# Optimization experiments

Measured on AMD Instinct MI355X. Metric: run time of the kernel, lower is better.

## Reference

```python
import jax, jax.numpy as jnp
import numpy as np

S = 32          # input grid resolution
N = 2048        # active input voxels
C = 256         # in channels
CO = 128        # out channels
S2 = 2 * S      # upsampled resolution
M = 8 * N       # candidate child voxels
EPS = 1e-6


def setup_inputs() -> dict:
    key = jax.random.key(0)
    ks = jax.random.split(key, 8)
    # unique voxel coordinates (sparse occupancy)
    lin = jax.random.permutation(ks[0], S ** 3)[:N]
    coords = jnp.stack([lin // (S * S), (lin // S) % S, lin % S], axis=-1).astype(jnp.int32)
    sc = 0.05
    return {
        "feats": jax.random.normal(ks[1], (N, C), jnp.float32),
        "norm1_w": 1.0 + 0.1 * jax.random.normal(ks[2], (C,), jnp.float32),
        "norm1_b": 0.1 * jax.random.normal(ks[3], (C,), jnp.float32),
        "subdiv_w": sc * jax.random.normal(ks[4], (C, 8), jnp.float32),
        "subdiv_b": jnp.zeros((8,), jnp.float32),
        "conv1_w": sc * jax.random.normal(ks[5], (27, C, CO), jnp.float32),
        "conv1_b": jnp.zeros((CO,), jnp.float32),
        "conv2_w": sc * jax.random.normal(ks[6], (27, CO, CO), jnp.float32),
        "conv2_b": jnp.zeros((CO,), jnp.float32),
        "skip_w": sc * jax.random.normal(ks[7], (C, CO), jnp.float32),
        "skip_b": jnp.zeros((CO,), jnp.float32),
        "coords": coords,
    }


def _layernorm(x, w=None, b=None):
    # LayerNorm32: fp32 math, eps=1e-6
    m = jnp.mean(x, axis=-1, keepdims=True)
    v = jnp.var(x, axis=-1, keepdims=True)
    y = (x - m) * jax.lax.rsqrt(v + EPS)
    if w is not None:
        y = y * w + b
    return y


def _sparse_conv(feats, nidx, w, b):
    # submanifold 3x3x3 sparse conv: gather 27 neighbors, contract.
    # nidx: [M,27] with sentinel M pointing at a zero row.
    pad = jnp.concatenate([feats, jnp.zeros((1, feats.shape[1]), feats.dtype)], axis=0)
    g = pad[nidx]                                   # [M, 27, Cin]
    return jnp.einsum('nkc,kcd->nd', g, w) + b


def _forward(feats, norm1_w, norm1_b, subdiv_w, subdiv_b, conv1_w, conv1_b,
             conv2_w, conv2_b, skip_w, skip_b, coords):
    # subdiv prediction (SparseLinear C -> 8)
    subdiv = feats @ subdiv_w + subdiv_b            # [N, 8]
    # norm1 + silu
    h = jax.nn.silu(_layernorm(feats, norm1_w, norm1_b))
    # sparse upsample x2 with octree subdivision mask
    mask = (subdiv > 0).reshape(-1)                 # [M]
    j = jnp.arange(8, dtype=jnp.int32)
    offs8 = jnp.stack([(j >> 2) & 1, (j >> 1) & 1, j & 1], axis=-1)  # [8,3]
    cc = (coords[:, None, :] * 2 + offs8[None]).reshape(-1, 3)        # [M,3]
    h_c = jnp.where(mask[:, None], jnp.repeat(h, 8, axis=0), 0.0)     # [M,C]
    x_c = jnp.where(mask[:, None], jnp.repeat(feats, 8, axis=0), 0.0)
    # neighbor lookup grid (padded by 1; default M -> zero feature row)
    grid = jnp.full((S2 + 2, S2 + 2, S2 + 2), M, jnp.int32)
    grid = grid.at[cc[:, 0] + 1, cc[:, 1] + 1, cc[:, 2] + 1].set(
        jnp.arange(M, dtype=jnp.int32))
    d = jnp.arange(-1, 2, dtype=jnp.int32)
    offs27 = jnp.stack(jnp.meshgrid(d, d, d, indexing='ij'), axis=-1).reshape(27, 3)
    nc = cc[:, None, :] + 1 + offs27[None]          # [M,27,3]
    nidx = grid[nc[..., 0], nc[..., 1], nc[..., 2]] # [M,27]
    # conv1 -> norm2 (no affine) -> silu -> conv2
    h1 = jax.nn.silu(_layernorm(_sparse_conv(h_c, nidx, conv1_w, conv1_b)))
    h2 = _sparse_conv(h1, nidx, conv2_w, conv2_b)
    # residual with linear skip; mask out non-subdivided children
    out = (h2 + x_c @ skip_w + skip_b) * mask[:, None].astype(h2.dtype)
    return out, subdiv


def reference(feats, norm1_w, norm1_b, subdiv_w, subdiv_b, conv1_w, conv1_b,
              conv2_w, conv2_b, skip_w, skip_b, coords):
    return _forward(feats, norm1_w, norm1_b, subdiv_w, subdiv_b, conv1_w,
                    conv1_b, conv2_w, conv2_b, skip_w, skip_b, coords)
```

## Files before the change

kernel.cpp:

```cpp
#include <hip/hip_runtime.h>
#include <cstdint>
#include <cstddef>

constexpr int N  = 2048;
constexpr int C  = 256;
constexpr int CO = 128;
constexpr int M  = 16384;
constexpr int G  = 66;
constexpr int KP = 6;
constexpr int KCHUNK = 5;
constexpr float EPS = 1e-6f;

using bf8 = __attribute__((ext_vector_type(8))) short;
using f4  = __attribute__((ext_vector_type(4))) float;

static __device__ __forceinline__ unsigned short f2bf(float f) {
  unsigned u = __float_as_uint(f);
  u += 0x7fffu + ((u >> 16) & 1u);
  return (unsigned short)(u >> 16);
}
static __device__ __forceinline__ float bf2f(unsigned short s) {
  return __uint_as_float((unsigned)s << 16);
}

__global__ __launch_bounds__(256) void k_prep(
    const float* __restrict__ c1w, unsigned short* __restrict__ w1t,
    const float* __restrict__ c2w, unsigned short* __restrict__ w2t,
    int* __restrict__ grid, unsigned short* __restrict__ h,
    unsigned short* __restrict__ h1) {
  int i = blockIdx.x * 256 + threadIdx.x;
  if (i < G * G * G) grid[i] = M;
  if (blockIdx.x == 1200) {
    if (threadIdx.x < C) h[(size_t)N * C + threadIdx.x] = 0;
  }
  if (blockIdx.x == 1201) {
    if (threadIdx.x < CO) h1[(size_t)M * CO + threadIdx.x] = 0;
  }

  __shared__ float tile[32][33];
  int bx = blockIdx.x;
  const float* w; unsigned short* wtp; int cin, k, cb, ob;
  if (bx < 864) {
    w = c1w; wtp = w1t; cin = C;
    k = bx >> 5; int tl = bx & 31; cb = tl >> 2; ob = tl & 3;
  } else {
    int b2 = bx - 864;
    w = c2w; wtp = w2t; cin = CO;
    k = b2 >> 4; int tl = b2 & 15; cb = tl >> 2; ob = tl & 3;
  }
  int ty = threadIdx.x >> 5, tx = threadIdx.x & 31;
#pragma unroll
  for (int j = 0; j < 4; ++j) {
    int row = ty + j * 8;
    tile[row][tx] = w[((size_t)k * cin + cb * 32 + row) * CO + ob * 32 + tx];
  }
  __syncthreads();
#pragma unroll
  for (int j = 0; j < 4; ++j) {
    int row = ty + j * 8;
    wtp[((size_t)k * CO + ob * 32 + row) * cin + cb * 32 + tx] =
        f2bf(tile[tx][row]);
  }
}

__global__ __launch_bounds__(256) void k_rownorm(
    const float* __restrict__ feats, const float* __restrict__ n1w,
    const float* __restrict__ n1b, const float* __restrict__ sdw,
    const float* __restrict__ sdb, float* __restrict__ out_subdiv,
    unsigned short* __restrict__ h, int* __restrict__ pidx,
    float* __restrict__ maskf, const int* __restrict__ coords,
    int* __restrict__ grid, const float* __restrict__ skw,
    const float* __restrict__ skb, float* __restrict__ sres) {
  int n = blockIdx.x, t = threadIdx.x;
  __shared__ float sx[256];
  __shared__ float sacc[256];
  float x = feats[(size_t)n * C + t];
  sx[t] = x;
  float4 w0 = *(const float4*)(sdw + t * 8);
  float4 w1 = *(const float4*)(sdw + t * 8 + 4);
  float v[10] = {x * w0.x, x * w0.y, x * w0.z, x * w0.w,
                 x * w1.x, x * w1.y, x * w1.z, x * w1.w, x, x * x};
#pragma unroll
  for (int mk = 1; mk < 64; mk <<= 1) {
#pragma unroll
    for (int j = 0; j < 10; ++j) v[j] += __shfl_xor(v[j], mk, 64);
  }
  __shared__ float red[4][10];
  int wave = t >> 6, lane = t & 63;
  if (lane == 0) {
#pragma unroll
    for (int j = 0; j < 10; ++j) red[wave][j] = v[j];
  }
  __syncthreads();
  float sums[10];
#pragma unroll
  for (int j = 0; j < 10; ++j)
    sums[j] = red[0][j] + red[1][j] + red[2][j] + red[3][j];
  float mean = sums[8] / (float)C;
  float var  = sums[9] / (float)C - mean * mean;
  float rstd = rsqrtf(var + EPS);
  if (t < 8) {
    float sd = sums[t] + sdb[t];
    out_subdiv[(size_t)n * 8 + t] = sd;
    bool mk = sd > 0.f;
    pidx[n * 8 + t]  = mk ? n : N;
    maskf[n * 8 + t] = mk ? 1.f : 0.f;
    int xx = coords[n * 3 + 0] * 2 + ((t >> 2) & 1) + 1;
    int yy = coords[n * 3 + 1] * 2 + ((t >> 1) & 1) + 1;
    int zz = coords[n * 3 + 2] * 2 + (t & 1) + 1;
    grid[(xx * G + yy) * G + zz] = n * 8 + t;
  }
  float y  = (x - mean) * rstd * n1w[t] + n1b[t];
  float sl = y / (1.f + __expf(-y));
  h[(size_t)n * C + t] = f2bf(sl);

  int o = t & 127, half = t >> 7;
  const float* wp = skw + (size_t)(half * 128) * CO + o;
  const float* xs = sx + half * 128;
  float a = 0.f;
#pragma unroll 8
  for (int c = 0; c < 128; ++c) a += xs[c] * wp[(size_t)c * CO];
  sacc[t] = a;
  __syncthreads();
  if (t < 128) sres[(size_t)n * CO + t] = sacc[t] + sacc[t + 128] + skb[t];
}

template <int CIN, int NCB, bool UP>
__global__ __launch_bounds__(256, 3) void k_conv(
    const unsigned short* __restrict__ src, const int* __restrict__ coords,
    const int* __restrict__ grid, const int* __restrict__ pidx,
    const unsigned short* __restrict__ wt, unsigned short* __restrict__ part) {
  __shared__ unsigned short sB[2][128 * 32];
  const int t = threadIdx.x;
  const int w = t >> 6, lane = t & 63;
  const int quad = lane >> 4, ln = lane & 15;
  const int m0 = blockIdx.x * 128;
  const int kpart = blockIdx.y;
  const int k0 = kpart * KCHUNK;
  const int nk = min(KCHUNK, 27 - k0);
  const int nstage = nk * NCB;
  const int rh = (w >> 1) * 64, ch = (w & 1) * 64;

  const int row2 = t >> 1;
  const int c0 = (t & 1) * 2;
  const int x3 = (row2 >> 1) & 3;
  const int wsl0 = row2 * 32 + ((c0) ^ x3) * 8;
  const int wsl1 = row2 * 32 + ((c0 + 1) ^ x3) * 8;
  const int slot = (quad ^ ((ln >> 1) & 3)) * 8;

  int gb[4];
#pragma unroll
  for (int ti = 0; ti < 4; ++ti) {
    int m = m0 + rh + ti * 16 + ln;
    int p = m >> 3, j = m & 7;
    int cx = coords[p * 3 + 0] * 2 + ((j >> 2) & 1) + 1;
    int cy = coords[p * 3 + 1] * 2 + ((j >> 1) & 1) + 1;
    int cz = coords[p * 3 + 2] * 2 + (j & 1) + 1;
    gb[ti] = (cx * G + cy) * G + cz;
  }
  auto tapoff = [&](int k) {
    return (k / 9 - 1) * (G * G) + ((k / 3) % 3 - 1) * G + (k % 3 - 1);
  };
  auto lookup = [&](int ti, int doff) {
    int g = grid[gb[ti] + doff];
    if (UP) return (g >= M) ? N : pidx[g & (M - 1)];
    return g;
  };

  bf8 rb0, rb1;
  bf8 ra[4], rn[4];
  int ga[4], gn[4];

  auto loadB = [&](int s) {
    const int kk = s / NCB, cb = s - kk * NCB;
    const unsigned short* pb =
        wt + ((size_t)(k0 + kk) * CO + row2) * CIN + cb * 32 + c0 * 8;
    rb0 = *(const bf8*)(pb);
    rb1 = *(const bf8*)(pb + 8);
  };
  auto writeB = [&](int buf) {
    *(bf8*)(sB[buf] + wsl0) = rb0;
    *(bf8*)(sB[buf] + wsl1) = rb1;
  };

  f4 acc[16];
  f4 zero = {0.f, 0.f, 0.f, 0.f};
#pragma unroll
  for (int i = 0; i < 16; ++i) acc[i] = zero;

  {
    int d0 = tapoff(k0);
#pragma unroll
    for (int ti = 0; ti < 4; ++ti) ga[ti] = lookup(ti, d0);
  }
  loadB(0);
#pragma unroll
  for (int ti = 0; ti < 4; ++ti)
    ra[ti] = *(const bf8*)(src + (size_t)ga[ti] * CIN + quad * 8);
  writeB(0);

  for (int s = 0; s < nstage; ++s) {
    const int buf = s & 1;
    const int kk = s / NCB, cb = s - kk * NCB;
    const bool have = (s + 1 < nstage);
    if (cb == 0 && kk + 1 < nk) {
      int dn = tapoff(k0 + kk + 1);
#pragma unroll
      for (int ti = 0; ti < 4; ++ti) gn[ti] = lookup(ti, dn);
    }
    if (have) {
      loadB(s + 1);
      const int cb1 = (cb + 1 < NCB) ? cb + 1 : 0;
      const int* gu = (cb + 1 < NCB) ? ga : gn;
#pragma unroll
      for (int ti = 0; ti < 4; ++ti)
        rn[ti] = *(const bf8*)(src + (size_t)gu[ti] * CIN + cb1 * 32 + quad * 8);
    }
    __syncthreads();
    const unsigned short* pb = sB[buf];
    bf8 bv[4];
#pragma unroll
    for (int tj = 0; tj < 4; ++tj)
      bv[tj] = *(const bf8*)(pb + (ch + tj * 16 + ln) * 32 + slot);
#pragma unroll
    for (int ti = 0; ti < 4; ++ti)
#pragma unroll
      for (int tj = 0; tj < 4; ++tj)
        acc[ti * 4 + tj] = __builtin_amdgcn_mfma_f32_16x16x32_bf16(
            ra[ti], bv[tj], acc[ti * 4 + tj], 0, 0, 0);
    if (have) {
      writeB(buf ^ 1);
#pragma unroll
      for (int ti = 0; ti < 4; ++ti) ra[ti] = rn[ti];
      if (cb + 1 == NCB) {
#pragma unroll
        for (int ti = 0; ti < 4; ++ti) ga[ti] = gn[ti];
      }
    }
  }

  unsigned short* pp = part + ((size_t)kpart * M + m0) * CO;
#pragma unroll
  for (int ti = 0; ti < 4; ++ti) {
    int mrow = rh + ti * 16 + quad * 4;
#pragma unroll
    for (int tj = 0; tj < 4; ++tj) {
      int co = ch + tj * 16 + ln;
#pragma unroll
      for (int rr = 0; rr < 4; ++rr)
        pp[(size_t)(mrow + rr) * CO + co] = f2bf(acc[ti * 4 + tj][rr]);
    }
  }
}

__global__ __launch_bounds__(256) void k_r1(const unsigned short* __restrict__ p,
                                            const float* __restrict__ bias,
                                            unsigned short* __restrict__ h1) {
  int wave = threadIdx.x >> 6, lane = threadIdx.x & 63;
  int m = blockIdx.x * 4 + wave;
  float v0 = bias[lane], v1 = bias[lane + 64];
#pragma unroll
  for (int q = 0; q < KP; ++q) {
    const unsigned short* pq = p + ((size_t)q * M + m) * CO;
    v0 += bf2f(pq[lane]);
    v1 += bf2f(pq[lane + 64]);
  }
  float sum = v0 + v1, sq = v0 * v0 + v1 * v1;
#pragma unroll
  for (int mk = 1; mk < 64; mk <<= 1) {
    sum += __shfl_xor(sum, mk, 64);
    sq  += __shfl_xor(sq, mk, 64);
  }
  float mean = sum / (float)CO;
  float var  = sq / (float)CO - mean * mean;
  float rstd = rsqrtf(var + EPS);
  float y0 = (v0 - mean) * rstd;
  float y1 = (v1 - mean) * rstd;
  float s0 = y0 / (1.f + __expf(-y0));
  float s1 = y1 / (1.f + __expf(-y1));
  h1[(size_t)m * CO + lane]      = f2bf(s0);
  h1[(size_t)m * CO + lane + 64] = f2bf(s1);
}

__global__ __launch_bounds__(256) void k_r2(const unsigned short* __restrict__ p,
                                            const float* __restrict__ bias,
                                            const float* __restrict__ sres,
                                            const float* __restrict__ maskf,
                                            float* __restrict__ out) {
  int i = blockIdx.x * 256 + threadIdx.x;
  int m = i >> 5;
  int o4 = (i & 31) * 4;
  float4 acc = *(const float4*)(bias + o4);
#pragma unroll
  for (int q = 0; q < KP; ++q) {
    ushort4 a = *(const ushort4*)(p + ((size_t)q * M + m) * CO + o4);
    acc.x += bf2f(a.x); acc.y += bf2f(a.y);
    acc.z += bf2f(a.z); acc.w += bf2f(a.w);
  }
  float4 s = *(const float4*)(sres + (size_t)(m >> 3) * CO + o4);
  float mk = maskf[m];
  float4 r;
  r.x = (acc.x + s.x) * mk;
  r.y = (acc.y + s.y) * mk;
  r.z = (acc.z + s.z) * mk;
  r.w = (acc.w + s.w) * mk;
  *(float4*)(out + (size_t)m * CO + o4) = r;
}

extern "C" void kernel_launch(void* const* d_in, const int* in_sizes, int n_in,
                              void* d_out, int out_size, void* d_ws, size_t ws_size,
                              hipStream_t stream) {
  const float* feats = (const float*)d_in[0];
  const float* n1w   = (const float*)d_in[1];
  const float* n1b   = (const float*)d_in[2];
  const float* sdw   = (const float*)d_in[3];
  const float* sdb   = (const float*)d_in[4];
  const float* c1w   = (const float*)d_in[5];
  const float* c1b   = (const float*)d_in[6];
  const float* c2w   = (const float*)d_in[7];
  const float* c2b   = (const float*)d_in[8];
  const float* skw   = (const float*)d_in[9];
  const float* skb   = (const float*)d_in[10];
  const int* coords  = (const int*)d_in[11];
  float* out = (float*)d_out;

  char* ws = (char*)d_ws;
  size_t off = 0;
  auto alloc = [&](size_t bytes) -> char* {
    char* p = ws + off;
    off += (bytes + 255) & ~(size_t)255;
    return p;
  };
  unsigned short* h    = (unsigned short*)alloc((size_t)(N + 1) * C * 2);
  unsigned short* h1   = (unsigned short*)alloc((size_t)(M + 1) * CO * 2);
  int*   grid  = (int*)alloc((size_t)G * G * G * 4);
  int*   pidx  = (int*)alloc((size_t)M * 4);
  float* maskf = (float*)alloc((size_t)M * 4);
  float* sres  = (float*)alloc((size_t)N * CO * 4);
  unsigned short* w1t = (unsigned short*)alloc((size_t)27 * CO * C * 2);
  unsigned short* w2t = (unsigned short*)alloc((size_t)27 * CO * CO * 2);
  unsigned short* pc  = (unsigned short*)alloc((size_t)KP * M * CO * 2);

  k_prep<<<1296, 256, 0, stream>>>(c1w, w1t, c2w, w2t, grid, h, h1);
  k_rownorm<<<N, 256, 0, stream>>>(feats, n1w, n1b, sdw, sdb,
                                   out + (size_t)M * CO, h, pidx, maskf,
                                   coords, grid, skw, skb, sres);

  k_conv<C, 8, true><<<dim3(M / 128, KP), 256, 0, stream>>>(h, coords, grid,
                                                            pidx, w1t, pc);
  k_r1<<<M / 4, 256, 0, stream>>>(pc, c1b, h1);

  k_conv<CO, 4, false><<<dim3(M / 128, KP), 256, 0, stream>>>(h1, coords, grid,
                                                              pidx, w2t, pc);
  k_r2<<<M * CO / 4 / 256, 256, 0, stream>>>(pc, c2b, sres, maskf, out);
}
```

Baseline: 193.8 us.

## Load conv weights directly into registers and interleave taps across K-partitions

Drops the LDS double-buffered weight tile and its per-stage __syncthreads. Each wave now loads its B fragments straight from global memory (L2-cached) into registers, alongside the gathered A rows. Taps are now spread across the 6 K-partitions with a stride of KP (3 partitions get 5 taps, 3 get 4) instead of contiguous chunks of 5. This removes block synchronisation and LDS traffic, but each weight element is now fetched once per wave pair instead of once per block, which raises global load volume and register pressure.

```diff
diff --git a/kernel.cpp b/kernel.cpp
--- a/kernel.cpp
+++ b/kernel.cpp
@@ -8,7 +8,6 @@
 constexpr int M  = 16384;
 constexpr int G  = 66;
 constexpr int KP = 6;
-constexpr int KCHUNK = 5;
 constexpr float EPS = 1e-6f;
 
 using bf8 = __attribute__((ext_vector_type(8))) short;
@@ -130,23 +129,14 @@
     const unsigned short* __restrict__ src, const int* __restrict__ coords,
     const int* __restrict__ grid, const int* __restrict__ pidx,
     const unsigned short* __restrict__ wt, unsigned short* __restrict__ part) {
-  __shared__ unsigned short sB[2][128 * 32];
   const int t = threadIdx.x;
   const int w = t >> 6, lane = t & 63;
   const int quad = lane >> 4, ln = lane & 15;
   const int m0 = blockIdx.x * 128;
   const int kpart = blockIdx.y;
-  const int k0 = kpart * KCHUNK;
-  const int nk = min(KCHUNK, 27 - k0);
-  const int nstage = nk * NCB;
+  const int ntap = (kpart < 3) ? 5 : 4;
+  const int nstage = ntap * NCB;
   const int rh = (w >> 1) * 64, ch = (w & 1) * 64;
-
-  const int row2 = t >> 1;
-  const int c0 = (t & 1) * 2;
-  const int x3 = (row2 >> 1) & 3;
-  const int wsl0 = row2 * 32 + ((c0) ^ x3) * 8;
-  const int wsl1 = row2 * 32 + ((c0 + 1) ^ x3) * 8;
-  const int slot = (quad ^ ((ln >> 1) & 3)) * 8;
 
   int gb[4];
 #pragma unroll
@@ -167,20 +157,20 @@
     return g;
   };
 
-  bf8 rb0, rb1;
   bf8 ra[4], rn[4];
+  bf8 rb[4], rbn[4];
   int ga[4], gn[4];
 
-  auto loadB = [&](int s) {
-    const int kk = s / NCB, cb = s - kk * NCB;
-    const unsigned short* pb =
-        wt + ((size_t)(k0 + kk) * CO + row2) * CIN + cb * 32 + c0 * 8;
-    rb0 = *(const bf8*)(pb);
-    rb1 = *(const bf8*)(pb + 8);
-  };
-  auto writeB = [&](int buf) {
-    *(bf8*)(sB[buf] + wsl0) = rb0;
-    *(bf8*)(sB[buf] + wsl1) = rb1;
+  auto loadA = [&](bf8* dst, const int* g, int cb) {
+#pragma unroll
+    for (int ti = 0; ti < 4; ++ti)
+      dst[ti] = *(const bf8*)(src + (size_t)g[ti] * CIN + cb * 32 + quad * 8);
+  };
+  auto loadBf = [&](bf8* dst, int k, int cb) {
+#pragma unroll
+    for (int tj = 0; tj < 4; ++tj)
+      dst[tj] = *(const bf8*)(wt + ((size_t)k * CO + ch + tj * 16 + ln) * CIN +
+                              cb * 32 + quad * 8);
   };
 
   f4 acc[16];
@@ -189,49 +179,38 @@
   for (int i = 0; i < 16; ++i) acc[i] = zero;
 
   {
-    int d0 = tapoff(k0);
+    int d0 = tapoff(kpart);
 #pragma unroll
     for (int ti = 0; ti < 4; ++ti) ga[ti] = lookup(ti, d0);
   }
-  loadB(0);
-#pragma unroll
-  for (int ti = 0; ti < 4; ++ti)
-    ra[ti] = *(const bf8*)(src + (size_t)ga[ti] * CIN + quad * 8);
-  writeB(0);
+  loadA(ra, ga, 0);
+  loadBf(rb, kpart, 0);
 
   for (int s = 0; s < nstage; ++s) {
-    const int buf = s & 1;
     const int kk = s / NCB, cb = s - kk * NCB;
+    const int k = kpart + kk * KP;
     const bool have = (s + 1 < nstage);
-    if (cb == 0 && kk + 1 < nk) {
-      int dn = tapoff(k0 + kk + 1);
+    if (cb == 0 && kk + 1 < ntap) {
+      int dn = tapoff(k + KP);
 #pragma unroll
       for (int ti = 0; ti < 4; ++ti) gn[ti] = lookup(ti, dn);
     }
     if (have) {
-      loadB(s + 1);
       const int cb1 = (cb + 1 < NCB) ? cb + 1 : 0;
+      const int kn  = (cb + 1 < NCB) ? k : k + KP;
       const int* gu = (cb + 1 < NCB) ? ga : gn;
-#pragma unroll
-      for (int ti = 0; ti < 4; ++ti)
-        rn[ti] = *(const bf8*)(src + (size_t)gu[ti] * CIN + cb1 * 32 + quad * 8);
+      loadA(rn, gu, cb1);
+      loadBf(rbn, kn, cb1);
     }
-    __syncthreads();
-    const unsigned short* pb = sB[buf];
-    bf8 bv[4];
-#pragma unroll
-    for (int tj = 0; tj < 4; ++tj)
-      bv[tj] = *(const bf8*)(pb + (ch + tj * 16 + ln) * 32 + slot);
 #pragma unroll
     for (int ti = 0; ti < 4; ++ti)
 #pragma unroll
       for (int tj = 0; tj < 4; ++tj)
         acc[ti * 4 + tj] = __builtin_amdgcn_mfma_f32_16x16x32_bf16(
-            ra[ti], bv[tj], acc[ti * 4 + tj], 0, 0, 0);
+            ra[ti], rb[tj], acc[ti * 4 + tj], 0, 0, 0);
     if (have) {
-      writeB(buf ^ 1);
-#pragma unroll
-      for (int ti = 0; ti < 4; ++ti) ra[ti] = rn[ti];
+#pragma unroll
+      for (int i = 0; i < 4; ++i) { ra[i] = rn[i]; rb[i] = rbn[i]; }
       if (cb + 1 == NCB) {
 #pragma unroll
         for (int ti = 0; ti < 4; ++ti) ga[ti] = gn[ti];
```

Measured after the change: 240.9 us. 1.24x slower.
